# Kernel optimization log

Measured on AMD Instinct MI355X. Metric: run time of the kernel, lower is better.

## Reference

```python
import jax, jax.numpy as jnp
import numpy as np

# Static problem dims (all graphs equal-sized so adaptive pool = uniform bins)
B = 64          # graphs
N = 2048        # nodes per graph
E = 16          # node_emb_dim
H_OUT, W_OUT = 32, 4   # AdaptiveAvgPool2d output -> pooled_dim = 128
COND = 64       # cond_emb_dim
HID = 512       # mlp_h_dim
BN_EPS = 1e-5


def _lin_init(key, out_d, in_d):
    kw, kb = jax.random.split(key)
    lim = 1.0 / np.sqrt(in_d)
    W = jax.random.uniform(kw, (out_d, in_d), jnp.float32, -lim, lim)
    b = jax.random.uniform(kb, (out_d,), jnp.float32, -lim, lim)
    return W, b


def setup_inputs() -> dict:
    key = jax.random.key(0)
    ks = jax.random.split(key, 6)
    Ntot = B * N
    x = jax.random.normal(ks[0], (Ntot, E), jnp.float32)
    batch = jnp.repeat(jnp.arange(B, dtype=jnp.int32), N)  # sorted segment ids
    cond = jax.random.normal(ks[1], (Ntot, COND), jnp.float32)
    mlp_in = COND + H_OUT * W_OUT  # 192
    W1, b1 = _lin_init(ks[2], HID, mlp_in)
    W2, b2 = _lin_init(ks[3], HID, HID)
    W3, b3 = _lin_init(ks[4], 3, HID)
    g1 = jnp.ones((HID,), jnp.float32); be1 = jnp.zeros((HID,), jnp.float32)
    g2 = jnp.ones((HID,), jnp.float32); be2 = jnp.zeros((HID,), jnp.float32)
    return {"x": x, "batch": batch, "conditioner_z_ref": cond,
            "W1": W1, "b1": b1, "g1": g1, "be1": be1,
            "W2": W2, "b2": b2, "g2": g2, "be2": be2,
            "W3": W3, "b3": b3}


def _bn_gelu(h, g, be):
    # BatchNorm1d in training mode: biased batch stats over the node axis
    m = h.mean(axis=0)
    v = h.var(axis=0)
    h = g * (h - m) * jax.lax.rsqrt(v + BN_EPS) + be
    return jax.nn.gelu(h, approximate=False)


def reference(x, batch, conditioner_z_ref, W1, b1, g1, be1, W2, b2, g2, be2, W3, b3):
    # Per-graph adaptive avg pool: since N % H_OUT == 0 and E % W_OUT == 0,
    # AdaptiveAvgPool2d is exactly mean over uniform (N/H_OUT, E/W_OUT) bins.
    xb = x.reshape(B, H_OUT, N // H_OUT, W_OUT, E // W_OUT)
    batch_pooled = xb.mean(axis=(2, 4)).reshape(B, H_OUT * W_OUT)  # [B, 128]
    pooled_per_node = batch_pooled[batch]                           # gather to [Ntot, 128]
    h = jnp.concatenate([conditioner_z_ref, pooled_per_node], axis=1)  # [Ntot, 192]
    h = _bn_gelu(h @ W1.T + b1, g1, be1)
    h = _bn_gelu(h @ W2.T + b2, g2, be2)
    return h @ W3.T + b3  # [Ntot, 3] predicted coords
```

## Files before the change

### kernel.cpp

```cpp
#include <hip/hip_runtime.h>
#include <hip/hip_bf16.h>
#include <math.h>
#include <stdint.h>

#define B_GRAPHS 64
#define N_NODES  2048
#define E_DIM    16
#define M_TOT    (B_GRAPHS * N_NODES)
#define K_COND   64
#define MLP_IN   192
#define HID      512
#define POOLD    128
#define BN_EPS   1e-5f

typedef __attribute__((ext_vector_type(8))) short bfrag8;
typedef __attribute__((ext_vector_type(4))) float facc4;

__device__ __forceinline__ unsigned short f2b(float f) {
    unsigned int x = __builtin_bit_cast(unsigned int, f);
    unsigned int r = x + 0x7fffu + ((x >> 16) & 1u);
    return (unsigned short)(r >> 16);
}
__device__ __forceinline__ float b2f(unsigned short u) {
    unsigned int x = ((unsigned int)u) << 16;
    return __builtin_bit_cast(float, x);
}

__device__ __forceinline__ float gelu_fast(float y) {
    float x  = y * 0.70710678118654752440f;
    float ax = fabsf(x);
    float t  = __builtin_amdgcn_rcpf(fmaf(0.3275911f, ax, 1.0f));
    float p  = fmaf(1.061405429f, t, -1.453152027f);
    p = fmaf(p, t, 1.421413741f);
    p = fmaf(p, t, -0.284496736f);
    p = fmaf(p, t, 0.254829592f);
    p = p * t;
    float e = __expf(-x * x);
    float erfax = fmaf(-p, e, 1.0f);
    float erfx  = copysignf(erfax, x);
    return 0.5f * y * (1.0f + erfx);
}

#define GLOAD_LDS16(g, l)                                                        \
    __builtin_amdgcn_global_load_lds(                                            \
        (const __attribute__((address_space(1))) unsigned int*)(const void*)(g), \
        (__attribute__((address_space(3))) unsigned int*)(void*)(l), 16, 0, 0)

__global__ __launch_bounds__(512) void prep_kernel(const float* __restrict__ x,
                                                   const float* __restrict__ W1,
                                                   const float* __restrict__ b1,
                                                   float* __restrict__ gbias) {
    __shared__ float pl[POOLD];
    int g = blockIdx.x, t = threadIdx.x;
    if (t < 128) {
        int h = t >> 2, w = t & 3;
        const float* base = x + (size_t)g * N_NODES * E_DIM + (size_t)h * 64 * E_DIM + w * 4;
        float s = 0.f;
        #pragma unroll 4
        for (int r = 0; r < 64; ++r) {
            float4 v = *reinterpret_cast<const float4*>(base + (size_t)r * E_DIM);
            s += v.x + v.y + v.z + v.w;
        }
        pl[h * 4 + w] = s * (1.0f / 256.0f);
    }
    __syncthreads();
    const float* wr_ = W1 + (size_t)t * MLP_IN + K_COND;
    float s = b1[t];
    #pragma unroll 4
    for (int k = 0; k < POOLD; ++k) s = fmaf(pl[k], wr_[k], s);
    gbias[g * HID + t] = s;
}

__global__ __launch_bounds__(256) void cvt_kernel(const float* __restrict__ s,
                                                  unsigned short* __restrict__ d) {
    size_t i = ((size_t)blockIdx.x * 256 + threadIdx.x) * 8;
    float4 v0 = *reinterpret_cast<const float4*>(s + i);
    float4 v1 = *reinterpret_cast<const float4*>(s + i + 4);
    unsigned short t[8] = {f2b(v0.x), f2b(v0.y), f2b(v0.z), f2b(v0.w),
                           f2b(v1.x), f2b(v1.y), f2b(v1.z), f2b(v1.w)};
    *reinterpret_cast<bfrag8*>(d + i) = *reinterpret_cast<bfrag8*>(t);
}

__device__ __forceinline__ bfrag8 load_f32x8_as_bf16(const float* p) {
    float4 v0 = *reinterpret_cast<const float4*>(p);
    float4 v1 = *reinterpret_cast<const float4*>(p + 4);
    unsigned short t[8] = {f2b(v0.x), f2b(v0.y), f2b(v0.z), f2b(v0.w),
                           f2b(v1.x), f2b(v1.y), f2b(v1.z), f2b(v1.w)};
    return *reinterpret_cast<bfrag8*>(t);
}

__global__ __launch_bounds__(512, 2) void gemm1_kernel(const float* __restrict__ A,
                                                       const float* __restrict__ W,
                                                       const float* __restrict__ gbias,
                                                       float* __restrict__ sums,
                                                       unsigned short* __restrict__ C) {
    __shared__ float sArr[HID], qArr[HID];
    const int t = threadIdx.x;
    const int r0 = blockIdx.x * 128;
    const int g = r0 >> 11;
    const int l = t & 63, w = t >> 6;
    const int wr = w >> 2, wc = w & 3;
    const int ln = l & 15, kg = l >> 4;
    sArr[t] = 0.f; qArr[t] = 0.f;
    __syncthreads();

    facc4 acc[4][8];
    const facc4 z = {0.f, 0.f, 0.f, 0.f};
    #pragma unroll
    for (int a = 0; a < 4; ++a)
        #pragma unroll
        for (int b = 0; b < 8; ++b) acc[a][b] = z;

    #pragma unroll
    for (int ks = 0; ks < 2; ++ks) {
        bfrag8 af[4], bf[8];
        #pragma unroll
        for (int a = 0; a < 4; ++a)
            af[a] = load_f32x8_as_bf16(A + (size_t)(r0 + wr * 64 + a * 16 + ln) * K_COND + ks * 32 + kg * 8);
        #pragma unroll
        for (int b = 0; b < 8; ++b)
            bf[b] = load_f32x8_as_bf16(W + (size_t)(wc * 128 + b * 16 + ln) * MLP_IN + ks * 32 + kg * 8);
        #pragma unroll
        for (int a = 0; a < 4; ++a)
            #pragma unroll
            for (int b = 0; b < 8; ++b)
                acc[a][b] = __builtin_amdgcn_mfma_f32_16x16x32_bf16(af[a], bf[b], acc[a][b], 0, 0, 0);
    }

    const float* gb = gbias + (size_t)g * HID;
    float gbv[8];
    #pragma unroll
    for (int b = 0; b < 8; ++b) gbv[b] = gb[wc * 128 + b * 16 + ln];
    float cs[8], cq[8];
    #pragma unroll
    for (int b = 0; b < 8; ++b) { cs[b] = 0.f; cq[b] = 0.f; }
    #pragma unroll
    for (int a = 0; a < 4; ++a) {
        #pragma unroll
        for (int i = 0; i < 4; ++i) {
            size_t rbase = (size_t)(r0 + wr * 64 + a * 16 + kg * 4 + i) * HID + wc * 128 + ln;
            #pragma unroll
            for (int b = 0; b < 8; ++b) {
                float v = acc[a][b][i] + gbv[b];
                C[rbase + b * 16] = f2b(v);
                cs[b] += v; cq[b] = fmaf(v, v, cq[b]);
            }
        }
    }
    #pragma unroll
    for (int b = 0; b < 8; ++b) {
        cs[b] += __shfl_xor(cs[b], 16, 64); cq[b] += __shfl_xor(cq[b], 16, 64);
        cs[b] += __shfl_xor(cs[b], 32, 64); cq[b] += __shfl_xor(cq[b], 32, 64);
    }
    if (kg == 0) {
        #pragma unroll
        for (int b = 0; b < 8; ++b) {
            int cl = wc * 128 + b * 16 + ln;
            atomicAdd(&sArr[cl], cs[b]); atomicAdd(&qArr[cl], cq[b]);
        }
    }
    __syncthreads();
    atomicAdd(&sums[t], sArr[t]);
    atomicAdd(&sums[HID + t], qArr[t]);
}

__global__ __launch_bounds__(512, 2) void gemm2_kernel(const unsigned short* __restrict__ A,
                                                       const unsigned short* __restrict__ Bm,
                                                       const float* __restrict__ sums1,
                                                       const float* __restrict__ g1,
                                                       const float* __restrict__ be1,
                                                       const float* __restrict__ bias,
                                                       float* __restrict__ sums,
                                                       unsigned short* __restrict__ C) {
    __shared__ unsigned short As[2][128 * 32];
    __shared__ unsigned short Bs[2][512 * 32];
    __shared__ float lss[2 * HID];
    __shared__ float sArr[HID], qArr[HID];
    const int t = threadIdx.x;
    const int r0 = blockIdx.x * 128;
    const int l = t & 63, w = t >> 6;
    const int wr = w >> 2, wc = w & 3;
    const int ln = l & 15, kg = l >> 4;
    const int arow = t >> 2, aslot = t & 3;
    const int awslot = aslot ^ ((arow >> 1) & 3);
    const int rr = l >> 2, sp = l & 3;
    const int bss = sp ^ ((rr >> 1) & 3);

    {
        float mean = sums1[t] * (1.0f / M_TOT);
        float var  = sums1[HID + t] * (1.0f / M_TOT) - mean * mean;
        float sc   = g1[t] * rsqrtf(var + BN_EPS);
        lss[t] = sc;
        lss[HID + t] = be1[t] - mean * sc;
    }
    sArr[t] = 0.f; qArr[t] = 0.f;

    facc4 acc[4][8];
    const facc4 z = {0.f, 0.f, 0.f, 0.f};
    #pragma unroll
    for (int a = 0; a < 4; ++a)
        #pragma unroll
        for (int b = 0; b < 8; ++b) acc[a][b] = z;

    const unsigned short* aptr = A + (size_t)(r0 + arow) * HID + aslot * 8;

    auto actwrite = [&](bfrag8 va, int kk, int buf) {
        unsigned short tmp[8];
        #pragma unroll
        for (int j = 0; j < 8; ++j) {
            int col = kk + aslot * 8 + j;
            float xv = b2f((unsigned short)va[j]);
            tmp[j] = f2b(gelu_fast(fmaf(xv, lss[col], lss[HID + col])));
        }
        *reinterpret_cast<bfrag8*>(&As[buf][arow * 32 + awslot * 8]) = *reinterpret_cast<bfrag8*>(tmp);
    };
    auto stageB = [&](int kk, int buf) {
        #pragma unroll
        for (int c = 0; c < 4; ++c) {
            int chunk = w * 4 + c;
            const unsigned short* gb = Bm + (size_t)(chunk * 16 + rr) * HID + kk + bss * 8;
            GLOAD_LDS16(gb, &Bs[buf][chunk * 512]);
        }
    };
    auto dsread = [&](bfrag8* af, bfrag8* bf, int buf) {
        #pragma unroll
        for (int a = 0; a < 4; ++a) {
            int RA = wr * 64 + a * 16 + ln;
            af[a] = *reinterpret_cast<const bfrag8*>(&As[buf][RA * 32 + (kg ^ ((RA >> 1) & 3)) * 8]);
        }
        #pragma unroll
        for (int b = 0; b < 8; ++b) {
            int RB = wc * 128 + b * 16 + ln;
            bf[b] = *reinterpret_cast<const bfrag8*>(&Bs[buf][RB * 32 + (kg ^ ((RB >> 1) & 3)) * 8]);
        }
    };
    auto domfma = [&](bfrag8* af, bfrag8* bf) {
        #pragma unroll
        for (int a = 0; a < 4; ++a)
            #pragma unroll
            for (int b = 0; b < 8; ++b)
                acc[a][b] = __builtin_amdgcn_mfma_f32_16x16x32_bf16(af[a], bf[b], acc[a][b], 0, 0, 0);
    };

    __syncthreads();

    bfrag8 va_p, va_q;
    va_p = *reinterpret_cast<const bfrag8*>(aptr);
    stageB(0, 0);
    va_q = *reinterpret_cast<const bfrag8*>(aptr + 32);
    stageB(32, 1);
    asm volatile("s_waitcnt vmcnt(9)" ::: "memory");
    actwrite(va_p, 0, 0);
    va_p = va_q;
    asm volatile("s_waitcnt lgkmcnt(0)" ::: "memory");

    bfrag8 af[4], bf[8];
    #pragma unroll 2
    for (int tt = 0; tt < 14; ++tt) {
        const int cur = tt & 1, nxt = cur ^ 1;
        asm volatile("s_waitcnt vmcnt(4)" ::: "memory");
        __builtin_amdgcn_s_barrier();
        __builtin_amdgcn_sched_barrier(0);
        dsread(af, bf, cur);
        actwrite(va_p, (tt + 1) * 32, nxt);
        asm volatile("s_waitcnt lgkmcnt(0)" ::: "memory");
        __builtin_amdgcn_s_barrier();
        __builtin_amdgcn_sched_barrier(0);
        va_q = *reinterpret_cast<const bfrag8*>(aptr + (tt + 2) * 32);
        stageB((tt + 2) * 32, cur);
        domfma(af, bf);
        va_p = va_q;
    }
    {
        asm volatile("s_waitcnt vmcnt(4)" ::: "memory");
        __builtin_amdgcn_s_barrier();
        __builtin_amdgcn_sched_barrier(0);
        dsread(af, bf, 0);
        actwrite(va_p, 15 * 32, 1);
        asm volatile("s_waitcnt lgkmcnt(0)" ::: "memory");
        __builtin_amdgcn_s_barrier();
        __builtin_amdgcn_sched_barrier(0);
        domfma(af, bf);
    }
    {
        asm volatile("s_waitcnt vmcnt(0)" ::: "memory");
        __builtin_amdgcn_s_barrier();
        __builtin_amdgcn_sched_barrier(0);
        dsread(af, bf, 1);
        asm volatile("s_waitcnt lgkmcnt(0)" ::: "memory");
        domfma(af, bf);
    }

    float bb[8];
    #pragma unroll
    for (int b = 0; b < 8; ++b) bb[b] = bias[wc * 128 + b * 16 + ln];
    float cs[8], cq[8];
    #pragma unroll
    for (int b = 0; b < 8; ++b) { cs[b] = 0.f; cq[b] = 0.f; }
    #pragma unroll
    for (int a = 0; a < 4; ++a) {
        #pragma unroll
        for (int i = 0; i < 4; ++i) {
            size_t rbase = (size_t)(r0 + wr * 64 + a * 16 + kg * 4 + i) * HID + wc * 128 + ln;
            #pragma unroll
            for (int b = 0; b < 8; ++b) {
                float v = acc[a][b][i] + bb[b];
                C[rbase + b * 16] = f2b(v);
                cs[b] += v; cq[b] = fmaf(v, v, cq[b]);
            }
        }
    }
    #pragma unroll
    for (int b = 0; b < 8; ++b) {
        cs[b] += __shfl_xor(cs[b], 16, 64); cq[b] += __shfl_xor(cq[b], 16, 64);
        cs[b] += __shfl_xor(cs[b], 32, 64); cq[b] += __shfl_xor(cq[b], 32, 64);
    }
    if (kg == 0) {
        #pragma unroll
        for (int b = 0; b < 8; ++b) {
            int cl = wc * 128 + b * 16 + ln;
            atomicAdd(&sArr[cl], cs[b]); atomicAdd(&qArr[cl], cq[b]);
        }
    }
    __syncthreads();
    atomicAdd(&sums[t], sArr[t]);
    atomicAdd(&sums[HID + t], qArr[t]);
}

__global__ void finalize_kernel(const float* __restrict__ sums, const float* __restrict__ g,
                                const float* __restrict__ be, float* __restrict__ ss) {
    int n = threadIdx.x;
    float mean = sums[n] * (1.0f / M_TOT);
    float var = sums[HID + n] * (1.0f / M_TOT) - mean * mean;
    float sc = g[n] * rsqrtf(var + BN_EPS);
    ss[n] = sc;
    ss[HID + n] = be[n] - mean * sc;
}

__global__ __launch_bounds__(256) void g3_kernel(const unsigned short* __restrict__ H2,
                                                 const float* __restrict__ ss2,
                                                 const float* __restrict__ W3,
                                                 const float* __restrict__ b3,
                                                 float* __restrict__ out) {
    __shared__ float lss[2 * HID];
    __shared__ float lw3[3 * HID];
    int t = threadIdx.x;
    for (int i = t; i < 2 * HID; i += 256) lss[i] = ss2[i];
    for (int i = t; i < 3 * HID; i += 256) lw3[i] = W3[i];
    __syncthreads();
    int l = t & 63, w = t >> 6;
    int rsub = l >> 3, lk = l & 7;
    int row = blockIdx.x * 32 + w * 8 + rsub;
    const unsigned short* p = H2 + (size_t)row * HID;
    float o0 = 0.f, o1 = 0.f, o2 = 0.f;
    #pragma unroll
    for (int it = 0; it < 8; ++it) {
        int k = it * 64 + lk * 8;
        bfrag8 v = *reinterpret_cast<const bfrag8*>(p + k);
        #pragma unroll
        for (int j = 0; j < 8; ++j) {
            float x = b2f((unsigned short)v[j]);
            float y = fmaf(x, lss[k + j], lss[HID + k + j]);
            y = gelu_fast(y);
            o0 = fmaf(y, lw3[k + j], o0);
            o1 = fmaf(y, lw3[HID + k + j], o1);
            o2 = fmaf(y, lw3[2 * HID + k + j], o2);
        }
    }
    #pragma unroll
    for (int m = 1; m < 8; m <<= 1) {
        o0 += __shfl_xor(o0, m, 64);
        o1 += __shfl_xor(o1, m, 64);
        o2 += __shfl_xor(o2, m, 64);
    }
    if (lk == 0) {
        out[(size_t)row * 3 + 0] = o0 + b3[0];
        out[(size_t)row * 3 + 1] = o1 + b3[1];
        out[(size_t)row * 3 + 2] = o2 + b3[2];
    }
}

extern "C" void kernel_launch(void* const* d_in, const int* in_sizes, int n_in,
                              void* d_out, int out_size, void* d_ws, size_t ws_size,
                              hipStream_t stream) {
    const float* x     = (const float*)d_in[0];
    const float* cond  = (const float*)d_in[2];
    const float* W1    = (const float*)d_in[3];
    const float* b1    = (const float*)d_in[4];
    const float* g1    = (const float*)d_in[5];
    const float* be1   = (const float*)d_in[6];
    const float* W2    = (const float*)d_in[7];
    const float* b2    = (const float*)d_in[8];
    const float* g2    = (const float*)d_in[9];
    const float* be2   = (const float*)d_in[10];
    const float* W3    = (const float*)d_in[11];
    const float* b3    = (const float*)d_in[12];

    const size_t H_BYTES = (size_t)M_TOT * HID * 2;
    if (ws_size < 2 * H_BYTES) return;
    char* ws = (char*)d_ws;
    unsigned short* H1 = (unsigned short*)ws;
    unsigned short* H2 = (unsigned short*)(ws + H_BYTES);

    float* outf   = (float*)d_out;
    float* gbias  = outf;
    float* sums1  = gbias + B_GRAPHS * HID;
    float* sums2  = sums1 + 2 * HID;
    unsigned short* W2bf = (unsigned short*)(sums2 + 2 * HID);
    float* ss2 = (float*)ws;

    hipMemsetAsync(sums1, 0, 2 * 2 * HID * sizeof(float), stream);

    prep_kernel<<<B_GRAPHS, 512, 0, stream>>>(x, W1, b1, gbias);
    cvt_kernel<<<(HID * HID / 8) / 256, 256, 0, stream>>>(W2, W2bf);

    gemm1_kernel<<<dim3(M_TOT / 128, 1), 512, 0, stream>>>(
        cond, W1, gbias, sums1, H1);

    gemm2_kernel<<<dim3(M_TOT / 128, 1), 512, 0, stream>>>(
        H1, W2bf, sums1, g1, be1, b2, sums2, H2);

    finalize_kernel<<<1, HID, 0, stream>>>(sums2, g2, be2, ss2);

    g3_kernel<<<M_TOT / 32, 256, 0, stream>>>(H2, ss2, W3, b3, outf);
}
```

Baseline: 297.8 us.

## Triple-buffer B tiles in gemm2 with a single barrier per k-step

Moves gemm2's B operand staging from double to triple buffering in LDS with rotating pointers. This allows one barrier per k-iteration instead of two, and the next global loads are issued right after that barrier. MFMA issue is wrapped in s_setprio. Both GEMM kernels drop launch_bounds min-blocks from 2 to 1, which frees registers but can lower occupancy. The larger LDS footprint, together with the removed unrolling and sched_barriers, may change scheduling and occupancy.

```diff
diff --git a/kernel.cpp b/kernel.cpp
--- a/kernel.cpp
+++ b/kernel.cpp
@@ -89,7 +89,7 @@
     return *reinterpret_cast<bfrag8*>(t);
 }
 
-__global__ __launch_bounds__(512, 2) void gemm1_kernel(const float* __restrict__ A,
+__global__ __launch_bounds__(512, 1) void gemm1_kernel(const float* __restrict__ A,
                                                        const float* __restrict__ W,
                                                        const float* __restrict__ gbias,
                                                        float* __restrict__ sums,
@@ -164,7 +164,7 @@
     atomicAdd(&sums[HID + t], qArr[t]);
 }
 
-__global__ __launch_bounds__(512, 2) void gemm2_kernel(const unsigned short* __restrict__ A,
+__global__ __launch_bounds__(512, 1) void gemm2_kernel(const unsigned short* __restrict__ A,
                                                        const unsigned short* __restrict__ Bm,
                                                        const float* __restrict__ sums1,
                                                        const float* __restrict__ g1,
@@ -173,7 +173,7 @@
                                                        float* __restrict__ sums,
                                                        unsigned short* __restrict__ C) {
     __shared__ unsigned short As[2][128 * 32];
-    __shared__ unsigned short Bs[2][512 * 32];
+    __shared__ unsigned short Bs[3][512 * 32];
     __shared__ float lss[2 * HID];
     __shared__ float sArr[HID], qArr[HID];
     const int t = threadIdx.x;
@@ -204,7 +204,7 @@
 
     const unsigned short* aptr = A + (size_t)(r0 + arow) * HID + aslot * 8;
 
-    auto actwrite = [&](bfrag8 va, int kk, int buf) {
+    auto actwrite = [&](bfrag8 va, int kk, unsigned short* asb) {
         unsigned short tmp[8];
         #pragma unroll
         for (int j = 0; j < 8; ++j) {
@@ -212,83 +212,66 @@
             float xv = b2f((unsigned short)va[j]);
             tmp[j] = f2b(gelu_fast(fmaf(xv, lss[col], lss[HID + col])));
         }
-        *reinterpret_cast<bfrag8*>(&As[buf][arow * 32 + awslot * 8]) = *reinterpret_cast<bfrag8*>(tmp);
+        *reinterpret_cast<bfrag8*>(&asb[arow * 32 + awslot * 8]) = *reinterpret_cast<bfrag8*>(tmp);
     };
-    auto stageB = [&](int kk, int buf) {
+    auto stageB = [&](int kk, unsigned short* bsb) {
         #pragma unroll
         for (int c = 0; c < 4; ++c) {
             int chunk = w * 4 + c;
             const unsigned short* gb = Bm + (size_t)(chunk * 16 + rr) * HID + kk + bss * 8;
-            GLOAD_LDS16(gb, &Bs[buf][chunk * 512]);
+            GLOAD_LDS16(gb, &bsb[chunk * 512]);
         }
     };
-    auto dsread = [&](bfrag8* af, bfrag8* bf, int buf) {
+
+    __syncthreads();
+
+    bfrag8 va_p, va_q;
+    va_p = *reinterpret_cast<const bfrag8*>(aptr);
+    stageB(0, Bs[0]);
+    va_q = *reinterpret_cast<const bfrag8*>(aptr + 32);
+    stageB(32, Bs[1]);
+    asm volatile("s_waitcnt vmcnt(9)" ::: "memory");
+    actwrite(va_p, 0, As[0]);
+    va_p = va_q;
+    asm volatile("s_waitcnt lgkmcnt(0)" ::: "memory");
+
+    unsigned short* bs_r  = Bs[0];
+    unsigned short* bs_n1 = Bs[1];
+    unsigned short* bs_n2 = Bs[2];
+    unsigned short* as_r  = As[0];
+    unsigned short* as_w  = As[1];
+
+    for (int tt = 0; tt < 16; ++tt) {
+        if (tt < 15) asm volatile("s_waitcnt vmcnt(4)" ::: "memory");
+        else         asm volatile("s_waitcnt vmcnt(0)" ::: "memory");
+        __builtin_amdgcn_s_barrier();
+        if (tt < 14) {
+            va_q = *reinterpret_cast<const bfrag8*>(aptr + (tt + 2) * 32);
+            stageB((tt + 2) * 32, bs_n2);
+        }
+        bfrag8 af[4], bf[8];
         #pragma unroll
         for (int a = 0; a < 4; ++a) {
             int RA = wr * 64 + a * 16 + ln;
-            af[a] = *reinterpret_cast<const bfrag8*>(&As[buf][RA * 32 + (kg ^ ((RA >> 1) & 3)) * 8]);
+            af[a] = *reinterpret_cast<const bfrag8*>(&as_r[RA * 32 + (kg ^ ((RA >> 1) & 3)) * 8]);
         }
         #pragma unroll
         for (int b = 0; b < 8; ++b) {
             int RB = wc * 128 + b * 16 + ln;
-            bf[b] = *reinterpret_cast<const bfrag8*>(&Bs[buf][RB * 32 + (kg ^ ((RB >> 1) & 3)) * 8]);
-        }
-    };
-    auto domfma = [&](bfrag8* af, bfrag8* bf) {
+            bf[b] = *reinterpret_cast<const bfrag8*>(&bs_r[RB * 32 + (kg ^ ((RB >> 1) & 3)) * 8]);
+        }
+        if (tt < 15) actwrite(va_p, (tt + 1) * 32, as_w);
+        __builtin_amdgcn_s_setprio(1);
         #pragma unroll
         for (int a = 0; a < 4; ++a)
             #pragma unroll
             for (int b = 0; b < 8; ++b)
                 acc[a][b] = __builtin_amdgcn_mfma_f32_16x16x32_bf16(af[a], bf[b], acc[a][b], 0, 0, 0);
-    };
-
-    __syncthreads();
-
-    bfrag8 va_p, va_q;
-    va_p = *reinterpret_cast<const bfrag8*>(aptr);
-    stageB(0, 0);
-    va_q = *reinterpret_cast<const bfrag8*>(aptr + 32);
-    stageB(32, 1);
-    asm volatile("s_waitcnt vmcnt(9)" ::: "memory");
-    actwrite(va_p, 0, 0);
-    va_p = va_q;
-    asm volatile("s_waitcnt lgkmcnt(0)" ::: "memory");
-
-    bfrag8 af[4], bf[8];
-    #pragma unroll 2
-    for (int tt = 0; tt < 14; ++tt) {
-        const int cur = tt & 1, nxt = cur ^ 1;
-        asm volatile("s_waitcnt vmcnt(4)" ::: "memory");
-        __builtin_amdgcn_s_barrier();
-        __builtin_amdgcn_sched_barrier(0);
-        dsread(af, bf, cur);
-        actwrite(va_p, (tt + 1) * 32, nxt);
+        __builtin_amdgcn_s_setprio(0);
         asm volatile("s_waitcnt lgkmcnt(0)" ::: "memory");
-        __builtin_amdgcn_s_barrier();
-        __builtin_amdgcn_sched_barrier(0);
-        va_q = *reinterpret_cast<const bfrag8*>(aptr + (tt + 2) * 32);
-        stageB((tt + 2) * 32, cur);
-        domfma(af, bf);
         va_p = va_q;
-    }
-    {
-        asm volatile("s_waitcnt vmcnt(4)" ::: "memory");
-        __builtin_amdgcn_s_barrier();
-        __builtin_amdgcn_sched_barrier(0);
-        dsread(af, bf, 0);
-        actwrite(va_p, 15 * 32, 1);
-        asm volatile("s_waitcnt lgkmcnt(0)" ::: "memory");
-        __builtin_amdgcn_s_barrier();
-        __builtin_amdgcn_sched_barrier(0);
-        domfma(af, bf);
-    }
-    {
-        asm volatile("s_waitcnt vmcnt(0)" ::: "memory");
-        __builtin_amdgcn_s_barrier();
-        __builtin_amdgcn_sched_barrier(0);
-        dsread(af, bf, 1);
-        asm volatile("s_waitcnt lgkmcnt(0)" ::: "memory");
-        domfma(af, bf);
+        unsigned short* tmpb = bs_r; bs_r = bs_n1; bs_n1 = bs_n2; bs_n2 = tmpb;
+        unsigned short* tmpa = as_r; as_r = as_w; as_w = tmpa;
     }
 
     float bb[8];
```

After: 291.9 us. 2.0% less time.
